# Kernel optimization log

Measured on AMD Instinct MI355X. Metric: run time of the kernel, lower is better.

## Reference

```python
import jax, jax.numpy as jnp
import numpy as np

N_WAY = 5
K_SHOT = 1
PROJ_DIM = 64
TEMPERATURE = 0.2
EPS_COS = 1e-12   # F.normalize eps in InnerproductSimilarity (cosine)
EPS_L2 = 1e-16    # _l2norm eps


def setup_inputs() -> dict:
    key = jax.random.key(0)
    ks = jax.random.split(key, 8)
    b, q, u, c, h, w = 2, 15, 20, 64, 21, 21
    s = N_WAY * K_SHOT
    std = float(np.sqrt(2.0 / PROJ_DIM))  # kaiming init used for 1x1 conv heads
    return {
        "support_xf": jax.random.normal(ks[0], (b, s, c, h, w), jnp.float32),
        "support_y": jax.random.randint(ks[1], (b, s), 0, N_WAY),
        "query_xf": jax.random.normal(ks[2], (b, q, c, h, w), jnp.float32),
        "query_y": jax.random.randint(ks[3], (b, q), 0, N_WAY),
        "unlabeled_xf": jax.random.normal(ks[4], (b, u, c, h, w), jnp.float32),
        "key_w": jax.random.normal(ks[5], (PROJ_DIM, c), jnp.float32) * std,
        "query_w": jax.random.normal(ks[6], (PROJ_DIM, c), jnp.float32) * std,
        "value_w": jax.random.normal(ks[7], (PROJ_DIM, c), jnp.float32) * std,
    }


def _dual_nn_selection(support_xf, unlabeled_xf):
    """Mutual-NN (dual NN) selection of unlabeled positions per class.
    Returns padded gather indices idx [b,n_way,L], 0/1 validity sel [b,n_way,L], and L.
    L is data-dependent (max per-(batch,class) count), computed eagerly like the
    original torch code's umask_length."""
    b, u, c, h, w = unlabeled_xf.shape
    M_u, M_s = u * h * w, K_SHOT * h * w
    unl = jnp.transpose(unlabeled_xf, (0, 2, 1, 3, 4)).reshape(b, c, M_u)  # [b,c,M_u]
    sup = jnp.transpose(support_xf.reshape(b, N_WAY, K_SHOT, c, h, w), (0, 1, 3, 2, 4, 5)).reshape(b, N_WAY, c, M_s)
    # cosine InnerproductSimilarity: normalize over channel dim
    sup_n = sup / jnp.maximum(jnp.linalg.norm(sup, axis=2, keepdims=True), EPS_COS)
    unl_n = unl / jnp.maximum(jnp.linalg.norm(unl, axis=1, keepdims=True), EPS_COS)
    u2s = jnp.einsum('bcm,bncs->bnms', unl_n, sup_n)  # [b,n_way,M_u,M_s]
    flat = jnp.transpose(u2s, (0, 2, 1, 3)).reshape(b, M_u, N_WAY * M_s)
    s_near = jnp.argmax(flat, axis=1)   # [b, n_way*M_s] nearest unlabeled pos per support slot
    u_near = jnp.argmax(flat, axis=2)   # [b, M_u] nearest support slot per unlabeled pos
    mutual = (jnp.take_along_axis(s_near, u_near, axis=1) == jnp.arange(M_u)[None, :])  # [b,M_u]
    cls = jnp.argmax(jnp.max(u2s, axis=-1), axis=1)  # [b,M_u] class assignment
    umask = jnp.transpose(jax.nn.one_hot(cls, N_WAY, dtype=jnp.float32), (0, 2, 1)) \
            * mutual[:, None, :].astype(jnp.float32)  # [b,n_way,M_u]
    L = int(jnp.max(jnp.sum(umask, axis=-1)))  # umask_length (data-dependent)
    order = jnp.argsort(-umask, axis=-1)       # stable: selected positions first, original order
    idx = order[:, :, :L]                      # [b,n_way,L]
    sel = jnp.take_along_axis(umask, idx, axis=-1)  # 1 = real feature, 0 = zero padding
    return idx, sel, L


def _forward_core(support_xf, query_xf, unlabeled_xf, key_w, query_w, value_w, query_y, idx, sel):
    b, q, c, h, w = query_xf.shape
    hw = h * w
    u = unlabeled_xf.shape[1]
    M_u, M_s = u * hw, K_SHOT * hw
    unl = jnp.transpose(unlabeled_xf, (0, 2, 1, 3, 4)).reshape(b, c, M_u)
    sup = jnp.transpose(support_xf.reshape(b, N_WAY, K_SHOT, c, h, w), (0, 1, 3, 2, 4, 5)).reshape(b, N_WAY, c, M_s)
    # ragged per-class scatter realized as padded gather (zeros where sel==0)
    gathered = jnp.take_along_axis(unl[:, None, :, :], idx[:, :, None, :], axis=-1)  # [b,n_way,c,L]
    unl_dual = gathered * sel[:, :, None, :]
    s_cat_u = jnp.concatenate([sup, unl_dual], axis=-1)  # [b,n_way,c,M_s+L]
    # 1x1 conv heads == channel matmuls
    qf = query_xf.reshape(b, q, c, hw)
    q_proj = jnp.einsum('oc,bqcm->bqom', query_w, qf)   # [b,q,64,hw]
    v_query = jnp.einsum('oc,bqcm->bqom', value_w, qf)  # [b,q,64,hw]
    k_sup = jnp.einsum('oc,bncl->bnol', key_w, s_cat_u)
    v_sup = jnp.einsum('oc,bncl->bnol', value_w, s_cat_u)
    simi = jnp.einsum('bqom,bnol->bqnml', q_proj, k_sup) / np.float32(np.sqrt(PROJ_DIM))  # [b,q,n,hw,Ms+L]
    Lt = simi.shape[-1]
    # _MNN with compensate_for_single == False (encoder == 'FourLayer_64F')
    merged = jnp.transpose(simi, (0, 1, 3, 2, 4)).reshape(b, q, hw, N_WAY * Lt)
    q_near = jnp.argmax(merged, axis=-1)  # [b,q,hw]
    s_near = jnp.argmax(merged, axis=-2)  # [b,q,n_way*Lt]
    q_mask = (jnp.take_along_axis(s_near, q_near, axis=-1) == jnp.arange(hw)[None, None, :]).astype(simi.dtype)
    att = jax.nn.softmax(simi * q_mask[:, :, None, :, None], axis=-1)
    aligned = jnp.einsum('bqnml,bnol->bqnmo', att, v_sup)  # [b,q,n_way,hw,64]
    aligned = aligned / (jnp.linalg.norm(aligned, axis=-1, keepdims=True) + EPS_L2)
    vq = v_query / (jnp.linalg.norm(v_query, axis=2, keepdims=True) + EPS_L2)
    simi2 = (jnp.einsum('bqnmo,bqok->bqnmk', aligned, vq) + 1.0) * 0.5  # FourLayer_64F rescale
    logits = jnp.sum(jnp.max(simi2, axis=-2), axis=-1).reshape(b * q, N_WAY)  # topk(1,-2)+mean == max
    logp = jax.nn.log_softmax(logits / np.float32(TEMPERATURE), axis=-1)
    y = query_y.reshape(b * q)
    return -jnp.mean(jnp.take_along_axis(logp, y[:, None], axis=1))  # CrossEntropyLoss


def reference(support_xf, support_y, query_xf, query_y, unlabeled_xf, key_w, query_w, value_w):
    idx, sel, _ = _dual_nn_selection(support_xf, unlabeled_xf)
    return _forward_core(support_xf, query_xf, unlabeled_xf, key_w, query_w, value_w, query_y, idx, sel)
```

## Files before the change

### kernel.cpp

```cpp
#include <hip/hip_runtime.h>
#include <math.h>

#define B 2
#define Q 15
#define U 20
#define C 64
#define HW 441
#define NW 5
#define MU (U*HW)
#define MS HW
#define NJ (NW*MS)
#define PD 64
#define LCAP NJ
#define LTCAP 896
#define SCAP 896
#define MSP 448
#define MUP 8832
#define NJP 2304
#define NEGF (-3.402823466e38f)

__device__ unsigned long long g_snearpack[B*NJ];
__device__ unsigned long long g_unearpack[B*MU];
__device__ int   g_counts[B*NW];
__device__ int   g_L[1];
__device__ int   g_selidx[B*NW*LCAP];
__device__ float g_unln[(size_t)B*C*MUP];
__device__ float g_supn[(size_t)B*C*NJP];
__device__ float g_ksup[(size_t)B*NW*PD*LTCAP];
__device__ float g_vsup[(size_t)B*NW*PD*LTCAP];
__device__ float g_vsupT[(size_t)B*NW*LTCAP*PD];
__device__ float g_vbarn[B*NW*PD];
__device__ float g_qproj[(size_t)B*Q*PD*MSP];
__device__ float g_vqn[(size_t)B*Q*PD*MSP];
__device__ unsigned long long g_rowpack[(size_t)B*Q*NW*MSP];
__device__ unsigned long long g_snear2pack[(size_t)B*Q*NW*LTCAP];
__device__ int   g_qmrows[B*Q*MSP];
__device__ int   g_qmcount[B*Q];
__device__ unsigned g_cmax[(size_t)B*Q*NW*MSP];
__device__ float g_logits[B*Q*NW];
__device__ float g_scores[(size_t)B*Q*NW*MSP*SCAP];

__device__ __forceinline__ unsigned enc_f(float f){
  unsigned b=__float_as_uint(f);
  return (b&0x80000000u)? ~b : (b|0x80000000u);
}
__device__ __forceinline__ float dec_f(unsigned k){
  unsigned b=(k&0x80000000u)?(k^0x80000000u):~k;
  return __uint_as_float(b);
}
__device__ __forceinline__ unsigned long long pk_make(float v,int idx){
  return ((unsigned long long)enc_f(v)<<32)|(unsigned)~(unsigned)idx;
}
__device__ __forceinline__ int pk_idx(unsigned long long p){
  return (int)~(unsigned)(p&0xFFFFFFFFull);
}

__global__ void k_init(){
  int i=blockIdx.x*256+threadIdx.x;
  if (i<B*NJ) g_snearpack[i]=0ull;
  if (i<B*MU) g_unearpack[i]=0ull;
  if (i<B*Q*NW*MSP){ g_rowpack[i]=0ull; g_cmax[i]=0u; }
  if (i<B*Q*NW*LTCAP) g_snear2pack[i]=0ull;
  if (i<B*C*(MUP-MU)){
    int b=i/(C*(MUP-MU)), r=i%(C*(MUP-MU)), c=r/(MUP-MU), m=MU+r%(MUP-MU);
    g_unln[((size_t)b*C+c)*MUP+m]=0.f;
  }
  if (i<B*C*(NJP-NJ)){
    int b=i/(C*(NJP-NJ)), r=i%(C*(NJP-NJ)), c=r/(NJP-NJ), j=NJ+r%(NJP-NJ);
    g_supn[((size_t)b*C+c)*NJP+j]=0.f;
  }
  if (i==0) g_L[0]=0;
}

__global__ void k_norms(const float* __restrict__ sup, const float* __restrict__ unl){
  int i=blockIdx.x*256+threadIdx.x;
  if (i<B*MU){
    int b=i/MU, m=i%MU, ui=m/HW, p=m%HW;
    const float* base=unl+((size_t)(b*U+ui)*C)*HW+p;
    float ss=0.f;
    for (int c=0;c<C;c++){ float x=base[(size_t)c*HW]; ss+=x*x; }
    float rn=1.f/fmaxf(sqrtf(ss),1e-12f);
    for (int c=0;c<C;c++) g_unln[((size_t)b*C+c)*MUP+m]=base[(size_t)c*HW]*rn;
  }
  if (i<B*NJ){
    int b=i/NJ, j=i%NJ, n=j/MS, s=j%MS;
    const float* base=sup+((size_t)(b*NW+n)*C)*HW+s;
    float ss=0.f;
    for (int c=0;c<C;c++){ float x=base[(size_t)c*HW]; ss+=x*x; }
    float rn=1.f/fmaxf(sqrtf(ss),1e-12f);
    for (int c=0;c<C;c++) g_supn[((size_t)b*C+c)*NJP+j]=base[(size_t)c*HW]*rn;
  }
}

__global__ __launch_bounds__(256) void k_u2s(){
  int blk=blockIdx.x;
  int jc=blk%18; blk/=18;
  int rb=blk%69; int b=blk/69;
  int m0=rb*128, j0=jc*128;
  int mv=min(128,MU-m0);
  int jv=min(128,NJ-j0);
  int tid=threadIdx.x, tm=tid>>4, tl=tid&15;
  int lane=tid&63, w=tid>>6;
  __shared__ __align__(16) float Ut[32*128];
  __shared__ __align__(16) float Pt[32*128];
  __shared__ unsigned long long colred[512];
  const size_t ub=(size_t)b*C*MUP+m0;
  const size_t pb=(size_t)b*C*NJP+j0;
  float s[8][8]={};
  #pragma unroll
  for (int h=0;h<2;h++){
    __syncthreads();
    for (int k4=tid;k4<1024;k4+=256){
      int c=k4>>5, mq=k4&31;
      *(float4*)&Ut[c*128+mq*4]=*(const float4*)&g_unln[ub+(size_t)(h*32+c)*MUP+mq*4];
      *(float4*)&Pt[c*128+mq*4]=*(const float4*)&g_supn[pb+(size_t)(h*32+c)*NJP+mq*4];
    }
    __syncthreads();
    for (int c=0;c<32;c++){
      float a[8],b0[4],b1[4];
      *(float4*)&a[0]=*(const float4*)&Ut[c*128+tm*8];
      *(float4*)&a[4]=*(const float4*)&Ut[c*128+tm*8+4];
      *(float4*)b0=*(const float4*)&Pt[c*128+tl*4];
      *(float4*)b1=*(const float4*)&Pt[c*128+64+tl*4];
      #pragma unroll
      for (int i=0;i<8;i++)
        #pragma unroll
        for (int j=0;j<4;j++){ s[i][j]=fmaf(a[i],b0[j],s[i][j]); s[i][j+4]=fmaf(a[i],b1[j],s[i][j+4]); }
    }
  }
  #pragma unroll
  for (int i=0;i<8;i++){
    int mm=tm*8+i;
    unsigned long long p=0ull;
    if (mm<mv){
      #pragma unroll
      for (int j=0;j<8;j++){
        int jj=(j<4)?(tl*4+j):(64+tl*4+(j-4));
        if (jj<jv){
          unsigned long long c2=pk_make(s[i][j],j0+jj);
          if (c2>p) p=c2;
        }
      }
    }
    #pragma unroll
    for (int mk=1;mk<16;mk<<=1){ unsigned long long o=__shfl_xor(p,mk); if (o>p) p=o; }
    if (tl==0 && mm<mv && p) atomicMax(&g_unearpack[b*MU+m0+mm],p);
  }
  #pragma unroll
  for (int j=0;j<8;j++){
    int jj=(j<4)?(tl*4+j):(64+tl*4+(j-4));
    unsigned long long p=0ull;
    #pragma unroll
    for (int i=0;i<8;i++){
      int mm=tm*8+i;
      if (mm<mv){
        unsigned long long c2=pk_make(s[i][j],m0+mm);
        if (c2>p) p=c2;
      }
    }
    {
      unsigned long long o=__shfl_xor(p,16); if (o>p) p=o;
      o=__shfl_xor(p,32); if (o>p) p=o;
    }
    if ((lane>>4)==0) colred[w*128+jj]=p;
  }
  __syncthreads();
  if (tid<128 && tid<jv){
    unsigned long long p=colred[tid];
    if (colred[128+tid]>p) p=colred[128+tid];
    if (colred[256+tid]>p) p=colred[256+tid];
    if (colred[384+tid]>p) p=colred[384+tid];
    if (p) atomicMax(&g_snearpack[b*NJ+j0+tid],p);
  }
}

__global__ __launch_bounds__(256) void k_compact(){
  int b=blockIdx.x/NW, n=blockIdx.x%NW;
  int tid=threadIdx.x, lane=tid&63, w=tid>>6;
  __shared__ int wtot[4];
  int base=0;
  for (int m0=0;m0<MU;m0+=256){
    int m=m0+tid;
    bool flag=false;
    if (m<MU){
      int j=pk_idx(g_unearpack[b*MU+m]);
      flag=(j/MS==n) && (pk_idx(g_snearpack[b*NJ+j])==m);
    }
    unsigned long long bal=__ballot(flag);
    if (lane==0) wtot[w]=(int)__popcll(bal);
    __syncthreads();
    int wpre=0, tot=0;
    #pragma unroll
    for (int ww=0;ww<4;ww++){ if (ww<w) wpre+=wtot[ww]; tot+=wtot[ww]; }
    if (flag){
      int pre=(int)__popcll(bal&((1ull<<lane)-1ull));
      g_selidx[(b*NW+n)*LCAP+base+wpre+pre]=m;
    }
    base+=tot;
    __syncthreads();
  }
  if (tid==0){ g_counts[b*NW+n]=base; atomicMax(&g_L[0],base); }
}

__global__ __launch_bounds__(256) void k_kv(const float* __restrict__ sup, const float* __restrict__ unl,
                                            const float* __restrict__ kw, const float* __restrict__ vw){
  int blk=blockIdx.x;
  int lb=blk%(LTCAP/64); blk/=(LTCAP/64);
  int n=blk%NW, b=blk/NW;
  int Lt=MS+g_L[0];
  if (lb*64>=Lt) return;
  int cnt=g_counts[b*NW+n];
  int tid=threadIdx.x, lane=tid&63, w=tid>>6;
  __shared__ float F[4096];
  __shared__ const float* ptr_s[64];
  if (tid<64){
    int l=lb*64+tid;
    const float* p=nullptr;
    if (l<MS) p=&sup[((size_t)(b*NW+n)*C)*HW+l];
    else if (l<MS+cnt){
      int mg=g_selidx[(b*NW+n)*LCAP+(l-MS)];
      int ui=mg/HW, pp=mg%HW;
      p=&unl[((size_t)(b*U+ui)*C)*HW+pp];
    }
    ptr_s[tid]=p;
  }
  __syncthreads();
  for (int k=tid;k<4096;k+=256){
    int c=k>>6, ll=k&63;
    const float* p=ptr_s[ll];
    F[c*64+ll]=p?p[(size_t)c*HW]:0.f;
  }
  __syncthreads();
  int l=lb*64+lane;
  size_t ob=((size_t)(b*NW+n)*PD)*LTCAP+l;
  size_t tb=((size_t)(b*NW+n)*LTCAP+l)*PD;
  for (int oo=0;oo<16;oo++){
    int o=w*16+oo;
    float ka=0.f, va=0.f;
    for (int c=0;c<C;c++){ float f=F[c*64+lane]; ka=fmaf(kw[o*C+c],f,ka); va=fmaf(vw[o*C+c],f,va); }
    g_ksup[ob+(size_t)o*LTCAP]=ka;
    g_vsup[ob+(size_t)o*LTCAP]=va;
    g_vsupT[tb+o]=va;
  }
}

__global__ __launch_bounds__(256) void k_vbar(){
  int bn=blockIdx.x;
  int tid=threadIdx.x, lane=tid&63, w=tid>>6;
  int cnt=g_counts[bn];
  int Lt=MS+g_L[0];
  __shared__ float vb_s[64];
  for (int oo=0;oo<16;oo++){
    int o=w*16+oo;
    const float* row=&g_vsup[((size_t)bn*PD+o)*LTCAP];
    float s=0.f;
    for (int l=lane;l<MS+cnt;l+=64) s+=row[l];
    #pragma unroll
    for (int mk=1;mk<64;mk<<=1) s+=__shfl_xor(s,mk);
    if (lane==0) vb_s[o]=s/(float)Lt;
  }
  __syncthreads();
  if (tid<64){
    float v=vb_s[tid];
    float ss=v*v;
    #pragma unroll
    for (int mk=1;mk<64;mk<<=1) ss+=__shfl_xor(ss,mk);
    g_vbarn[bn*PD+tid]=v/(sqrtf(ss)+1e-16f);
  }
}

__global__ __launch_bounds__(256) void k_qproj(const float* __restrict__ qx, const float* __restrict__ qw,
                                               const float* __restrict__ vw){
  int blk=blockIdx.x;
  int mt=blk%7; blk/=7;
  int bq=blk;
  int tid=threadIdx.x, lane=tid&63, w=tid>>6;
  __shared__ float F[4096];
  __shared__ float ssp[256];
  for (int k=tid;k<4096;k+=256){
    int c=k>>6, mm=k&63, m=mt*64+mm;
    F[c*64+mm]=(m<MS)?qx[((size_t)bq*C+c)*HW+m]:0.f;
  }
  __syncthreads();
  int m=mt*64+lane;
  size_t ob=(size_t)bq*PD*MSP+m;
  float va[16]; float ssl=0.f;
  for (int oo=0;oo<16;oo++){
    int o=w*16+oo;
    float qa=0.f, v=0.f;
    for (int c=0;c<C;c++){ float f=F[c*64+lane]; qa=fmaf(qw[o*C+c],f,qa); v=fmaf(vw[o*C+c],f,v); }
    g_qproj[ob+(size_t)o*MSP]=qa;
    va[oo]=v; ssl=fmaf(v,v,ssl);
  }
  ssp[tid]=ssl;
  __syncthreads();
  float ss=ssp[lane]+ssp[64+lane]+ssp[128+lane]+ssp[192+lane];
  float rn=1.f/(sqrtf(ss)+1e-16f);
  for (int oo=0;oo<16;oo++) g_vqn[ob+(size_t)(w*16+oo)*MSP]=va[oo]*rn;
}

__global__ __launch_bounds__(256) void k_passA(){
  int blk=blockIdx.x;
  int lc=blk%7; blk/=7;
  int mh=blk%4; blk/=4;
  int n=blk%NW; blk/=NW;
  int bq=blk; int b=bq/Q;
  int Lt=MS+g_L[0];
  int nch=(Lt+127)>>7;
  if (lc>=nch) return;
  int l0=lc<<7, lv=min(128,Lt-l0);
  int tid=threadIdx.x, tm=tid>>4, tl=tid&15;
  int lane=tid&63, w=tid>>6;
  int bqn=bq*NW+n;
  int m0=mh*128;
  __shared__ __align__(16) float Qt[32*128];
  __shared__ __align__(16) float Kt[32*128];
  __shared__ unsigned long long colred[512];
  const size_t qb=(size_t)bq*PD*MSP;
  const size_t kb=(size_t)(b*NW+n)*PD*LTCAP;
  float s[8][8]={};
  #pragma unroll
  for (int h=0;h<2;h++){
    __syncthreads();
    for (int k4=tid;k4<1024;k4+=256){
      int o=k4>>5, mq=k4&31;
      int m=m0+mq*4;
      float4 v=make_float4(0.f,0.f,0.f,0.f);
      if (m<MSP) v=*(const float4*)&g_qproj[qb+(size_t)(h*32+o)*MSP+m];
      *(float4*)&Qt[o*128+mq*4]=v;
      *(float4*)&Kt[o*128+mq*4]=*(const float4*)&g_ksup[kb+(size_t)(h*32+o)*LTCAP+l0+mq*4];
    }
    __syncthreads();
    for (int c=0;c<32;c++){
      float a[8],b0[4],b1[4];
      *(float4*)&a[0]=*(const float4*)&Qt[c*128+tm*8];
      *(float4*)&a[4]=*(const float4*)&Qt[c*128+tm*8+4];
      *(float4*)b0=*(const float4*)&Kt[c*128+tl*4];
      *(float4*)b1=*(const float4*)&Kt[c*128+64+tl*4];
      #pragma unroll
      for (int i=0;i<8;i++)
        #pragma unroll
        for (int j=0;j<4;j++){ s[i][j]=fmaf(a[i],b0[j],s[i][j]); s[i][j+4]=fmaf(a[i],b1[j],s[i][j+4]); }
    }
  }
  #pragma unroll
  for (int i=0;i<8;i++)
    #pragma unroll
    for (int j=0;j<8;j++) s[i][j]*=0.125f;
  #pragma unroll
  for (int i=0;i<8;i++){
    int m=m0+tm*8+i;
    if (m<MS){
      size_t sbase=((size_t)bqn*MSP+m)*SCAP+l0;
      *(float4*)&g_scores[sbase+tl*4]   =make_float4(s[i][0],s[i][1],s[i][2],s[i][3]);
      *(float4*)&g_scores[sbase+64+tl*4]=make_float4(s[i][4],s[i][5],s[i][6],s[i][7]);
    }
  }
  #pragma unroll
  for (int i=0;i<8;i++){
    int m=m0+tm*8+i;
    unsigned long long p=0ull;
    if (m<MS){
      #pragma unroll
      for (int j=0;j<8;j++){
        int jj=(j<4)?(tl*4+j):(64+tl*4+(j-4));
        if (jj<lv){
          unsigned long long c2=pk_make(s[i][j],l0+jj);
          if (c2>p) p=c2;
        }
      }
    }
    #pragma unroll
    for (int mk=1;mk<16;mk<<=1){ unsigned long long o=__shfl_xor(p,mk); if (o>p) p=o; }
    if (tl==0 && m<MS && p) atomicMax(&g_rowpack[(size_t)bqn*MSP+m],p);
  }
  #pragma unroll
  for (int j=0;j<8;j++){
    int jj=(j<4)?(tl*4+j):(64+tl*4+(j-4));
    unsigned long long p=0ull;
    #pragma unroll
    for (int i=0;i<8;i++){
      int m=m0+tm*8+i;
      if (m<MS){
        unsigned long long c2=pk_make(s[i][j],m);
        if (c2>p) p=c2;
      }
    }
    {
      unsigned long long o=__shfl_xor(p,16); if (o>p) p=o;
      o=__shfl_xor(p,32); if (o>p) p=o;
    }
    if ((lane>>4)==0) colred[w*128+jj]=p;
  }
  __syncthreads();
  if (tid<128 && tid<lv){
    unsigned long long p=colred[tid];
    if (colred[128+tid]>p) p=colred[128+tid];
    if (colred[256+tid]>p) p=colred[256+tid];
    if (colred[384+tid]>p) p=colred[384+tid];
    if (p) atomicMax(&g_snear2pack[(size_t)bqn*LTCAP+l0+tid],p);
  }
}

__global__ __launch_bounds__(256) void k_qmask(){
  int bq=blockIdx.x;
  int tid=threadIdx.x, lane=tid&63, w=tid>>6;
  __shared__ int wtot[4];
  int base=0;
  for (int m0=0;m0<MS;m0+=256){
    int m=m0+tid;
    bool qm=false;
    if (m<MS){
      unsigned bhv=0u; unsigned long long bp=0ull; int bn=0;
      #pragma unroll
      for (int n=0;n<NW;n++){
        unsigned long long pk=g_rowpack[(size_t)(bq*NW+n)*MSP+m];
        unsigned hv=(unsigned)(pk>>32);
        if (hv>bhv){bhv=hv;bp=pk;bn=n;}
      }
      int bl=pk_idx(bp);
      qm=(pk_idx(g_snear2pack[(size_t)(bq*NW+bn)*LTCAP+bl])==m);
    }
    unsigned long long bal=__ballot(qm);
    if (lane==0) wtot[w]=(int)__popcll(bal);
    __syncthreads();
    int wpre=0, tot=0;
    #pragma unroll
    for (int ww=0;ww<4;ww++){ if (ww<w) wpre+=wtot[ww]; tot+=wtot[ww]; }
    if (qm){
      int pre=(int)__popcll(bal&((1ull<<lane)-1ull));
      g_qmrows[bq*MSP+base+wpre+pre]=m;
    }
    base+=tot;
    __syncthreads();
  }
  if (tid==0) g_qmcount[bq]=base;
}

__global__ __launch_bounds__(256) void k_passB(){
  int blk=blockIdx.x;
  int rt=blk%7; blk/=7;
  int n=blk%NW; blk/=NW;
  int bq=blk; int b=bq/Q;
  int nm=g_qmcount[bq];
  if (rt*64>=nm) return;
  int bqn=bq*NW+n;
  int Lt=MS+g_L[0];
  int nch=(Lt+63)>>6;
  int tid=threadIdx.x, tm=tid>>4, tl=tid&15;
  __shared__ __align__(16) float Vt[4096];
  __shared__ __align__(16) float Pt[64*68];
  __shared__ int rows_s[64];
  if (tid<64){ int g=rt*64+tid; rows_s[tid]=(g<nm)?g_qmrows[bq*MSP+g]:0; }
  __syncthreads();
  float rmax[4]; size_t sb[4];
  #pragma unroll
  for (int i=0;i<4;i++){
    int row=rows_s[tm*4+i];
    rmax[i]=dec_f((unsigned)(g_rowpack[(size_t)bqn*MSP+row]>>32));
    sb[i]=((size_t)bqn*MSP+row)*SCAP;
  }
  const size_t vb=(size_t)(b*NW+n)*LTCAP*PD;
  const size_t qb=(size_t)bq*PD*MSP;
  float lsum[4]={0.f,0.f,0.f,0.f};
  float acc[4][4]={};
  for (int lc=0;lc<nch;lc++){
    int l0=lc<<6, lv=min(64,Lt-l0);
    __syncthreads();
    float4 sv[4];
    #pragma unroll
    for (int i=0;i<4;i++) sv[i]=*(const float4*)&g_scores[sb[i]+l0+tl*4];
    {
      const float* src=&g_vsupT[vb+(size_t)l0*PD];
      #pragma unroll
      for (int it=0;it<4;it++){
        int f4=tid+it*256;
        *(float4*)&Vt[f4*4]=*(const float4*)&src[f4*4];
      }
    }
    #pragma unroll
    for (int i=0;i<4;i++){
      float e0=(tl*4+0<lv)?__expf(sv[i].x-rmax[i]):0.f;
      float e1=(tl*4+1<lv)?__expf(sv[i].y-rmax[i]):0.f;
      float e2=(tl*4+2<lv)?__expf(sv[i].z-rmax[i]):0.f;
      float e3=(tl*4+3<lv)?__expf(sv[i].w-rmax[i]):0.f;
      lsum[i]+=(e0+e1)+(e2+e3);
      *(float4*)&Pt[(tm*4+i)*68+tl*4]=make_float4(e0,e1,e2,e3);
    }
    __syncthreads();
    for (int l4=0;l4<64;l4+=4){
      float4 pq[4];
      #pragma unroll
      for (int i=0;i<4;i++) pq[i]=*(const float4*)&Pt[(tm*4+i)*68+l4];
      #pragma unroll
      for (int u=0;u<4;u++){
        float4 v4=*(const float4*)&Vt[(l4+u)*64+tl*4];
        #pragma unroll
        for (int i=0;i<4;i++){
          float p=((const float*)&pq[i])[u];
          acc[i][0]=fmaf(p,v4.x,acc[i][0]);
          acc[i][1]=fmaf(p,v4.y,acc[i][1]);
          acc[i][2]=fmaf(p,v4.z,acc[i][2]);
          acc[i][3]=fmaf(p,v4.w,acc[i][3]);
        }
      }
    }
  }
  float rn[4];
  #pragma unroll
  for (int i=0;i<4;i++){
    float ls=lsum[i];
    #pragma unroll
    for (int mk=1;mk<16;mk<<=1) ls+=__shfl_xor(ls,mk);
    float ss=0.f;
    #pragma unroll
    for (int j=0;j<4;j++){ acc[i][j]/=ls; ss=fmaf(acc[i][j],acc[i][j],ss); }
    #pragma unroll
    for (int mk=1;mk<16;mk<<=1) ss+=__shfl_xor(ss,mk);
    rn[i]=1.f/(sqrtf(ss)+1e-16f);
  }
  __syncthreads();
  #pragma unroll
  for (int i=0;i<4;i++)
    *(float4*)&Pt[(tm*4+i)*68+tl*4]=make_float4(acc[i][0],acc[i][1],acc[i][2],acc[i][3]);
  int rowok[4];
  #pragma unroll
  for (int i=0;i<4;i++) rowok[i]=(rt*64+tm*4+i<nm);
  for (int kt=0;kt<7;kt++){
    __syncthreads();
    for (int k=tid;k<1024;k+=256){
      int o=k>>4, kq=k&15;
      *(float4*)&Vt[o*64+kq*4]=*(const float4*)&g_vqn[qb+(size_t)o*MSP+kt*64+kq*4];
    }
    __syncthreads();
    float d[4][4]={};
    for (int o=0;o<64;o++){
      float a[4], bv4[4];
      #pragma unroll
      for (int i=0;i<4;i++) a[i]=Pt[(tm*4+i)*68+o];
      *(float4*)bv4=*(const float4*)&Vt[o*64+tl*4];
      #pragma unroll
      for (int i=0;i<4;i++)
        #pragma unroll
        for (int j=0;j<4;j++) d[i][j]=fmaf(a[i],bv4[j],d[i][j]);
    }
    #pragma unroll
    for (int j=0;j<4;j++){
      int kg=kt*64+tl*4+j;
      float mv=NEGF;
      #pragma unroll
      for (int i=0;i<4;i++) if (rowok[i]) mv=fmaxf(mv,d[i][j]*rn[i]);
      mv=fmaxf(mv,__shfl_xor(mv,16));
      mv=fmaxf(mv,__shfl_xor(mv,32));
      if (((tid>>4)&3)==0 && kg<MS && mv>-1e37f)
        atomicMax(&g_cmax[(size_t)bqn*MSP+kg],enc_f(mv));
    }
  }
}

__global__ __launch_bounds__(256) void k_logits(){
  int bqn=blockIdx.x;
  int n=bqn%NW, bq=bqn/NW, b=bq/Q;
  int tid=threadIdx.x;
  int nm=g_qmcount[bq];
  __shared__ float red[256];
  __shared__ float vb_s[64];
  if (tid<64) vb_s[tid]=g_vbarn[(b*NW+n)*PD+tid];
  __syncthreads();
  const float* vq=&g_vqn[(size_t)bq*PD*MSP];
  float p=0.f;
  for (int k=tid;k<MS;k+=256){
    float v=dec_f(g_cmax[(size_t)bqn*MSP+k]);
    if (nm<MS){
      float d=0.f;
      for (int o=0;o<PD;o++) d=fmaf(vb_s[o],vq[(size_t)o*MSP+k],d);
      v=fmaxf(v,d);
    }
    p+=(v+1.f)*0.5f;
  }
  red[tid]=p; __syncthreads();
  for (int s=128;s;s>>=1){ if (tid<s) red[tid]+=red[tid+s]; __syncthreads(); }
  if (tid==0) g_logits[bqn]=red[0];
}

__global__ void k_loss(const int* __restrict__ qy, float* __restrict__ out){
  int t=threadIdx.x;
  float lp=0.f;
  if (t<B*Q){
    int y=qy[t];
    float xv[NW]; float mxv=NEGF;
    #pragma unroll
    for (int n=0;n<NW;n++){ xv[n]=g_logits[t*NW+n]*5.f; mxv=fmaxf(mxv,xv[n]); }
    float s=0.f, xy=0.f;
    #pragma unroll
    for (int n=0;n<NW;n++){ s+=__expf(xv[n]-mxv); if (n==y) xy=xv[n]; }
    lp=xy-mxv-logf(s);
  }
  #pragma unroll
  for (int off=32;off;off>>=1) lp+=__shfl_down(lp,off);
  if (t==0) out[0]=-lp/(float)(B*Q);
}

extern "C" void kernel_launch(void* const* d_in, const int* in_sizes, int n_in,
                              void* d_out, int out_size, void* d_ws, size_t ws_size,
                              hipStream_t stream) {
  (void)in_sizes; (void)n_in; (void)out_size; (void)d_ws; (void)ws_size;
  const float* sup=(const float*)d_in[0];
  const float* qx =(const float*)d_in[2];
  const int*   qy =(const int*)d_in[3];
  const float* unl=(const float*)d_in[4];
  const float* kw =(const float*)d_in[5];
  const float* qw =(const float*)d_in[6];
  const float* vw =(const float*)d_in[7];
  float* out=(float*)d_out;

  k_init   <<<525,256,0,stream>>>();
  k_norms  <<<69,256,0,stream>>>(sup,unl);
  k_u2s    <<<B*69*18,256,0,stream>>>();
  k_compact<<<B*NW,256,0,stream>>>();
  k_kv     <<<B*NW*(LTCAP/64),256,0,stream>>>(sup,unl,kw,vw);
  k_vbar   <<<B*NW,256,0,stream>>>();
  k_qproj  <<<B*Q*7,256,0,stream>>>(qx,qw,vw);
  k_passA  <<<B*Q*NW*28,256,0,stream>>>();
  k_qmask  <<<B*Q,256,0,stream>>>();
  k_passB  <<<B*Q*NW*7,256,0,stream>>>();
  k_logits <<<B*Q*NW,256,0,stream>>>();
  k_loss   <<<1,64,0,stream>>>(qy,out);
}
```

Measured before the change: 659.4 us.

## Register-prefetch next chunk of scores, V and query tiles in passB

```diff
diff --git a/kernel.cpp b/kernel.cpp
--- a/kernel.cpp
+++ b/kernel.cpp
@@ -437,7 +437,18 @@
   if (tid==0) g_qmcount[bq]=base;
 }
 
-__global__ __launch_bounds__(256) void k_passB(){
+#define EXPROW(i, svi) { \
+    float e0=(tl*4+0<lv)?__expf((svi).x-rmax[i]):0.f; \
+    float e1=(tl*4+1<lv)?__expf((svi).y-rmax[i]):0.f; \
+    float e2=(tl*4+2<lv)?__expf((svi).z-rmax[i]):0.f; \
+    float e3=(tl*4+3<lv)?__expf((svi).w-rmax[i]):0.f; \
+    lsum[i]+=(e0+e1)+(e2+e3); \
+    *(float4*)&Pt[(tm*4+(i))*68+tl*4]=make_float4(e0,e1,e2,e3); }
+#define KPLOAD(kp, it, ktv) { int kk=tid+(it)*256; int o=kk>>4, kq=kk&15; \
+    kp=*(const float4*)&g_vqn[qb+(size_t)o*MSP+(ktv)*64+kq*4]; }
+#define KPSTORE(kp, it) { int kk=tid+(it)*256; int o=kk>>4, kq=kk&15; \
+    *(float4*)&Vt[o*64+kq*4]=kp; }
+__global__ __launch_bounds__(256,4) void k_passB(){
   int blk=blockIdx.x;
   int rt=blk%7; blk/=7;
   int n=blk%NW; blk/=NW;
@@ -464,30 +475,39 @@
   const size_t qb=(size_t)bq*PD*MSP;
   float lsum[4]={0.f,0.f,0.f,0.f};
   float acc[4][4]={};
+  float4 sv0,sv1,sv2,sv3, vp0,vp1,vp2,vp3;
+  sv0=*(const float4*)&g_scores[sb[0]+tl*4];
+  sv1=*(const float4*)&g_scores[sb[1]+tl*4];
+  sv2=*(const float4*)&g_scores[sb[2]+tl*4];
+  sv3=*(const float4*)&g_scores[sb[3]+tl*4];
+  {
+    const float* src=&g_vsupT[vb];
+    vp0=*(const float4*)&src[(tid     )*4];
+    vp1=*(const float4*)&src[(tid+256 )*4];
+    vp2=*(const float4*)&src[(tid+512 )*4];
+    vp3=*(const float4*)&src[(tid+768 )*4];
+  }
   for (int lc=0;lc<nch;lc++){
     int l0=lc<<6, lv=min(64,Lt-l0);
     __syncthreads();
-    float4 sv[4];
-    #pragma unroll
-    for (int i=0;i<4;i++) sv[i]=*(const float4*)&g_scores[sb[i]+l0+tl*4];
-    {
-      const float* src=&g_vsupT[vb+(size_t)l0*PD];
-      #pragma unroll
-      for (int it=0;it<4;it++){
-        int f4=tid+it*256;
-        *(float4*)&Vt[f4*4]=*(const float4*)&src[f4*4];
-      }
-    }
-    #pragma unroll
-    for (int i=0;i<4;i++){
-      float e0=(tl*4+0<lv)?__expf(sv[i].x-rmax[i]):0.f;
-      float e1=(tl*4+1<lv)?__expf(sv[i].y-rmax[i]):0.f;
-      float e2=(tl*4+2<lv)?__expf(sv[i].z-rmax[i]):0.f;
-      float e3=(tl*4+3<lv)?__expf(sv[i].w-rmax[i]):0.f;
-      lsum[i]+=(e0+e1)+(e2+e3);
-      *(float4*)&Pt[(tm*4+i)*68+tl*4]=make_float4(e0,e1,e2,e3);
-    }
-    __syncthreads();
+    *(float4*)&Vt[(tid     )*4]=vp0;
+    *(float4*)&Vt[(tid+256 )*4]=vp1;
+    *(float4*)&Vt[(tid+512 )*4]=vp2;
+    *(float4*)&Vt[(tid+768 )*4]=vp3;
+    EXPROW(0,sv0) EXPROW(1,sv1) EXPROW(2,sv2) EXPROW(3,sv3)
+    __syncthreads();
+    if (lc+1<nch){
+      int l1=(lc+1)<<6;
+      sv0=*(const float4*)&g_scores[sb[0]+l1+tl*4];
+      sv1=*(const float4*)&g_scores[sb[1]+l1+tl*4];
+      sv2=*(const float4*)&g_scores[sb[2]+l1+tl*4];
+      sv3=*(const float4*)&g_scores[sb[3]+l1+tl*4];
+      const float* src=&g_vsupT[vb+(size_t)l1*PD];
+      vp0=*(const float4*)&src[(tid     )*4];
+      vp1=*(const float4*)&src[(tid+256 )*4];
+      vp2=*(const float4*)&src[(tid+512 )*4];
+      vp3=*(const float4*)&src[(tid+768 )*4];
+    }
     for (int l4=0;l4<64;l4+=4){
       float4 pq[4];
       #pragma unroll
@@ -506,6 +526,8 @@
       }
     }
   }
+  float4 kp0,kp1,kp2,kp3;
+  KPLOAD(kp0,0,0) KPLOAD(kp1,1,0) KPLOAD(kp2,2,0) KPLOAD(kp3,3,0)
   float rn[4];
   #pragma unroll
   for (int i=0;i<4;i++){
@@ -528,11 +550,11 @@
   for (int i=0;i<4;i++) rowok[i]=(rt*64+tm*4+i<nm);
   for (int kt=0;kt<7;kt++){
     __syncthreads();
-    for (int k=tid;k<1024;k+=256){
-      int o=k>>4, kq=k&15;
-      *(float4*)&Vt[o*64+kq*4]=*(const float4*)&g_vqn[qb+(size_t)o*MSP+kt*64+kq*4];
-    }
-    __syncthreads();
+    KPSTORE(kp0,0) KPSTORE(kp1,1) KPSTORE(kp2,2) KPSTORE(kp3,3)
+    __syncthreads();
+    if (kt+1<7){
+      KPLOAD(kp0,0,kt+1) KPLOAD(kp1,1,kt+1) KPLOAD(kp2,2,kt+1) KPLOAD(kp3,3,kt+1)
+    }
     float d[4][4]={};
     for (int o=0;o<64;o++){
       float a[4], bv4[4];
```

Result: no change. 652.3 us (median of 3 runs) (-1.1%).
